# Kernel tuning notes

Hardware: AMD Instinct MI355X
Metric: run time of the kernel (lower is better)

Reference implementation:

```python
import jax, jax.numpy as jnp
import numpy as np

S_LOCAL = 3
N_HEADS = 8
EPS = 1e-6


def setup_inputs() -> dict:
    key = jax.random.key(0)
    ks = jax.random.split(key, 9)
    B, D, T, H, W = 2, 512, 96, 16, 16
    std = 0.02
    return {
        "x": jax.random.normal(ks[0], (B, D, T, H, W), dtype=jnp.float32),
        "ln_gamma": jnp.ones((D,), dtype=jnp.float32),
        "ln_beta": jnp.zeros((D,), dtype=jnp.float32),
        "Wq": jax.random.normal(ks[1], (D, D), dtype=jnp.float32) * std,
        "Wk": jax.random.normal(ks[2], (D, D), dtype=jnp.float32) * std,
        "Wv": jax.random.normal(ks[3], (D, D), dtype=jnp.float32) * std,
        "Wkl": jax.random.normal(ks[4], (D, D), dtype=jnp.float32) * std,
        "Wvl": jax.random.normal(ks[5], (D, D), dtype=jnp.float32) * std,
        "Wo": jax.random.normal(ks[6], (D, D), dtype=jnp.float32) * std,
        "q_bias": jax.random.normal(ks[7], (1, N_HEADS, 1, D // N_HEADS), dtype=jnp.float32) * std,
    }


def _unfold_windows(x, s):
    # x: [..., T] -> [..., T, s] sliding windows with zero padding s//2 each side
    p = s // 2
    xp = jnp.pad(x, [(0, 0)] * (x.ndim - 1) + [(p, p)])
    T = x.shape[-1]
    idx = jnp.arange(T)[:, None] + jnp.arange(s)[None, :]  # [T, s]
    return xp[..., idx]


def reference(x, ln_gamma, ln_beta, Wq, Wk, Wv, Wkl, Wvl, Wo, q_bias):
    B, D, T, H, W = x.shape
    nh, dh, s = N_HEADS, D // N_HEADS, S_LOCAL
    factor = dh ** (-0.5)
    N = B * H * W

    # [B,D,T,H,W] -> [N, T, D]
    xt = jnp.transpose(x, (0, 3, 4, 2, 1)).reshape(N, T, D)

    # LayerNorm over D
    mu = xt.mean(-1, keepdims=True)
    var = xt.var(-1, keepdims=True)
    xn = (xt - mu) / jnp.sqrt(var + EPS) * ln_gamma + ln_beta

    # projections -> [N, nh, T, dh]
    def heads(y):
        return jnp.transpose(y.reshape(N, T, nh, dh), (0, 2, 1, 3))

    q = heads(xn @ Wq.T) + q_bias
    k = heads(xn @ Wk.T)
    v = heads(xn @ Wv.T)

    # global attention scores [N, nh, T, T]
    attn_global = jnp.einsum('bhnd,bhgd->bhng', q, k) * factor

    # local k/v: [N, T, D] -> [N, D, T] -> windows [N, D, T, s]
    kl = jnp.transpose(xn @ Wkl.T, (0, 2, 1))
    vl = jnp.transpose(xn @ Wvl.T, (0, 2, 1))
    k_w = jnp.transpose(_unfold_windows(kl, s).reshape(N, nh, dh, T, s), (0, 1, 3, 2, 4))  # [N,nh,T,dh,s]
    v_w = jnp.transpose(_unfold_windows(vl, s).reshape(N, nh, dh, T, s), (0, 1, 3, 2, 4))

    # local mask: True where window element came from zero padding -> [T, s]
    mask_local = _unfold_windows(jnp.ones((T,), dtype=jnp.float32), s) == 0

    attn_local = jnp.einsum('bhnd,bhndl->bhnl', q, k_w)
    attn_local = jnp.where(mask_local, -jnp.inf, attn_local) * factor

    # joint softmax over [T global + s local]
    attn_map = jax.nn.softmax(jnp.concatenate([attn_global, attn_local], axis=-1), axis=-1)
    ag, al = attn_map[..., :T], attn_map[..., T:]

    x_global = jnp.einsum('bhng,bhgd->bhnd', ag, v)
    x_local = jnp.einsum('bhnl,bhndl->bhnd', al, v_w)

    out = (jnp.transpose(x_global + x_local, (0, 2, 1, 3)).reshape(N, T, D)) @ Wo.T
    return jnp.transpose(out.reshape(B, H, W, T, D), (0, 4, 3, 1, 2))
```

## Files before the change

kernel.cpp:

```cpp
#include <hip/hip_runtime.h>
#include <hip/hip_fp16.h>
#include <cstdint>
#include <cstddef>

typedef _Float16 f16;
typedef _Float16 half8 __attribute__((ext_vector_type(8)));
typedef _Float16 half4v __attribute__((ext_vector_type(4)));
typedef float floatx4 __attribute__((ext_vector_type(4)));

#define MTOT 49152

__device__ __forceinline__ void gload_lds16(const f16* g, f16* l) {
  __builtin_amdgcn_global_load_lds((const __attribute__((address_space(1))) void*)g,
                                   (__attribute__((address_space(3))) void*)l, 16, 0, 0);
}

__device__ __forceinline__ half8 load_h8u(const f16* p) {
  half8 v;
  __builtin_memcpy(&v, p, 16);
  return v;
}

__global__ __launch_bounds__(256) void wconv_kernel(
    const float* __restrict__ Wq, const float* __restrict__ Wk,
    const float* __restrict__ Wv, const float* __restrict__ Wkl,
    const float* __restrict__ Wvl, const float* __restrict__ Wo,
    f16* __restrict__ WQKV, f16* __restrict__ WO) {
  int idx = blockIdx.x * 256 + threadIdx.x;
  if (idx < 2560 * 512) {
    int row = idx >> 9;
    int col = idx & 511;
    int seg = row >> 9;
    int r = row & 511;
    const float* src;
    switch (seg) {
      case 0: src = Wq; break;
      case 1: src = Wk; break;
      case 2: src = Wkl; break;
      case 3: src = Wvl; break;
      default: src = Wv; break;
    }
    WQKV[idx] = (f16)src[r * 512 + col];
  }
  if (idx < 512 * 512) WO[idx] = (f16)Wo[idx];
}

__global__ __launch_bounds__(256) void ln_kernel(
    const float* __restrict__ x, const float* __restrict__ gamma,
    const float* __restrict__ beta, f16* __restrict__ XN) {
  const int hwg = blockIdx.x & 3;
  const int t   = (blockIdx.x >> 2) % 96;
  const int b   = blockIdx.x / (4 * 96);
  const int lhw = threadIdx.x & 63;
  const int dg  = threadIdx.x >> 6;
  const int hw  = hwg * 64 + lhw;
  const float* xp = x + (size_t)b * 512 * 24576 + (size_t)t * 256 + hw;

  float s = 0.f, s2 = 0.f;
  for (int d = dg * 128; d < dg * 128 + 128; ++d) {
    float v = xp[(size_t)d * 24576];
    s += v;
    s2 += v * v;
  }
  __shared__ float S1[4][64], S2[4][64];
  S1[dg][lhw] = s;
  S2[dg][lhw] = s2;
  __syncthreads();
  s  = S1[0][lhw] + S1[1][lhw] + S1[2][lhw] + S1[3][lhw];
  s2 = S2[0][lhw] + S2[1][lhw] + S2[2][lhw] + S2[3][lhw];
  const float mean = s * (1.f / 512.f);
  float var = s2 * (1.f / 512.f) - mean * mean;
  var = fmaxf(var, 0.f);
  const float rstd = rsqrtf(var + 1e-6f);
  const int n = b * 256 + hw;
  f16* outp = XN + ((size_t)n * 96 + t) * 512;
  for (int d0 = dg * 128; d0 < dg * 128 + 128; d0 += 8) {
    half8 buf;
#pragma unroll
    for (int j = 0; j < 8; ++j) {
      float v = xp[(size_t)(d0 + j) * 24576];
      buf[j] = (f16)((v - mean) * rstd * gamma[d0 + j] + beta[d0 + j]);
    }
    *(half8*)(outp + d0) = buf;
  }
}

__global__ __launch_bounds__(512, 2) void gemmA_kernel(
    const f16* __restrict__ A, const f16* __restrict__ B,
    f16* __restrict__ Cqkv, const float* __restrict__ qbias) {
  __shared__ f16 LA[2][256 * 64];
  __shared__ f16 LB[2][256 * 64];
  __shared__ __align__(16) f16 esc[8][16][72];

  const int lin = blockIdx.x;
  const int cpx = (int)gridDim.x >> 3;
  const int swz = (lin & 7) * cpx + (lin >> 3);
  const int o = ((gridDim.x & 7) == 0) ? swz : lin;
  const int mt = o / 10;
  const int nt = o % 10;
  const int m0 = mt * 256;
  const int n0 = nt * 256;

  const int tid = threadIdx.x;
  const int wid = tid >> 6;
  const int lane = tid & 63;
  const int wm = wid >> 2;
  const int wn = wid & 3;
  const int l15 = lane & 15, l4 = lane >> 4;

  const int srow = tid >> 3;
  const int scol = ((tid & 7) ^ (srow & 7)) * 8;
  const f16* Abase = A + (size_t)(m0 + srow) * 512 + scol;
  const f16* Bbase = B + (size_t)(n0 + srow) * 512 + scol;

  const int cks0 = ((l4) ^ (l15 & 7)) * 8;
  const int cks1 = ((4 + l4) ^ (l15 & 7)) * 8;
  const int arow = wm * 128 + l15;
  const int brow = wn * 64 + l15;

  floatx4 acc[8][4] = {};
  half8 a_f[4][2];
  half8 b_f[4][2];

  auto stageH = [&](int slot, int kt, int mat, int h) {
    const f16* g = (mat ? Bbase : Abase) + kt * 64 + (size_t)(h * 128) * 512;
    f16* l = (mat ? LB[slot] : LA[slot]) + h * 8192 + tid * 8;
    gload_lds16(g, l);
    gload_lds16(g + (size_t)64 * 512, l + 4096);
  };

  stageH(0, 0, 0, 0); stageH(0, 0, 0, 1);
  stageH(0, 0, 1, 0); stageH(0, 0, 1, 1);
  stageH(1, 1, 0, 0); stageH(1, 1, 0, 1);
  asm volatile("s_waitcnt vmcnt(4)" ::: "memory");
  __builtin_amdgcn_s_barrier();

#pragma unroll
  for (int kt = 0; kt < 8; ++kt) {
    const f16* As = LA[kt & 1];
    const f16* Bs = LB[kt & 1];
    const int nsl = (kt + 1) & 1;

#pragma unroll
    for (int mf2 = 0; mf2 < 4; ++mf2) {
      a_f[mf2][0] = *(const half8*)(As + (arow + mf2 * 16) * 64 + cks0);
      a_f[mf2][1] = *(const half8*)(As + (arow + mf2 * 16) * 64 + cks1);
    }
#pragma unroll
    for (int nf = 0; nf < 2; ++nf) {
      b_f[nf][0] = *(const half8*)(Bs + (brow + nf * 16) * 64 + cks0);
      b_f[nf][1] = *(const half8*)(Bs + (brow + nf * 16) * 64 + cks1);
    }
    if (kt + 1 < 8) { stageH(nsl, kt + 1, 1, 0); stageH(nsl, kt + 1, 1, 1); }
    __builtin_amdgcn_s_barrier();
    __builtin_amdgcn_s_setprio(1);
#pragma unroll
    for (int mf2 = 0; mf2 < 4; ++mf2)
#pragma unroll
      for (int nf2 = 0; nf2 < 2; ++nf2)
#pragma unroll
        for (int ks = 0; ks < 2; ++ks)
          acc[mf2][nf2] = __builtin_amdgcn_mfma_f32_16x16x32_f16(
              a_f[mf2][ks], b_f[nf2][ks], acc[mf2][nf2], 0, 0, 0);
    __builtin_amdgcn_s_setprio(0);
    __builtin_amdgcn_s_barrier();

#pragma unroll
    for (int nf = 2; nf < 4; ++nf) {
      b_f[nf][0] = *(const half8*)(Bs + (brow + nf * 16) * 64 + cks0);
      b_f[nf][1] = *(const half8*)(Bs + (brow + nf * 16) * 64 + cks1);
    }
    __builtin_amdgcn_s_barrier();
    __builtin_amdgcn_s_setprio(1);
#pragma unroll
    for (int mf2 = 0; mf2 < 4; ++mf2)
#pragma unroll
      for (int nf2 = 0; nf2 < 2; ++nf2)
#pragma unroll
        for (int ks = 0; ks < 2; ++ks)
          acc[mf2][2 + nf2] = __builtin_amdgcn_mfma_f32_16x16x32_f16(
              a_f[mf2][ks], b_f[2 + nf2][ks], acc[mf2][2 + nf2], 0, 0, 0);
    __builtin_amdgcn_s_setprio(0);
    __builtin_amdgcn_s_barrier();

#pragma unroll
    for (int mf2 = 0; mf2 < 4; ++mf2) {
      a_f[mf2][0] = *(const half8*)(As + (arow + 64 + mf2 * 16) * 64 + cks0);
      a_f[mf2][1] = *(const half8*)(As + (arow + 64 + mf2 * 16) * 64 + cks1);
    }
    __builtin_amdgcn_s_barrier();
    __builtin_amdgcn_s_setprio(1);
#pragma unroll
    for (int mf2 = 0; mf2 < 4; ++mf2)
#pragma unroll
      for (int nf2 = 0; nf2 < 2; ++nf2)
#pragma unroll
        for (int ks = 0; ks < 2; ++ks)
          acc[4 + mf2][nf2] = __builtin_amdgcn_mfma_f32_16x16x32_f16(
              a_f[mf2][ks], b_f[nf2][ks], acc[4 + mf2][nf2], 0, 0, 0);
    __builtin_amdgcn_s_setprio(0);
    __builtin_amdgcn_s_barrier();

    if (kt + 2 < 8) { stageH(kt & 1, kt + 2, 0, 0); stageH(kt & 1, kt + 2, 0, 1); }
    __builtin_amdgcn_s_barrier();
    __builtin_amdgcn_s_setprio(1);
#pragma unroll
    for (int mf2 = 0; mf2 < 4; ++mf2)
#pragma unroll
      for (int nf2 = 0; nf2 < 2; ++nf2)
#pragma unroll
        for (int ks = 0; ks < 2; ++ks)
          acc[4 + mf2][2 + nf2] = __builtin_amdgcn_mfma_f32_16x16x32_f16(
              a_f[mf2][ks], b_f[2 + nf2][ks], acc[4 + mf2][2 + nf2], 0, 0, 0);
    __builtin_amdgcn_s_setprio(0);
    if (kt < 6) {
      asm volatile("s_waitcnt vmcnt(4)" ::: "memory");
    } else if (kt == 6) {
      asm volatile("s_waitcnt vmcnt(0)" ::: "memory");
    }
    __builtin_amdgcn_s_barrier();
  }

  float bias[4], scl[4];
#pragma unroll
  for (int nf = 0; nf < 4; ++nf) {
    const int n = n0 + wn * 64 + nf * 16 + l15;
    const bool isq = (n < 512);
    bias[nf] = isq ? qbias[n] : 0.0f;
    scl[nf]  = isq ? 0.125f : 1.0f;
  }
  const int rrow = lane >> 2;
  const int rcg  = lane & 3;
#pragma unroll
  for (int mf = 0; mf < 8; ++mf) {
#pragma unroll
    for (int nf = 0; nf < 4; ++nf)
#pragma unroll
      for (int j = 0; j < 4; ++j)
        esc[wid][l4 * 4 + j][nf * 16 + l15] = (f16)((acc[mf][nf][j] + bias[nf]) * scl[nf]);
    asm volatile("s_waitcnt lgkmcnt(0)" ::: "memory");
    half8 v0 = *(const half8*)(&esc[wid][rrow][rcg * 16]);
    half8 v1 = *(const half8*)(&esc[wid][rrow][rcg * 16 + 8]);
    asm volatile("" ::: "memory");
    f16* dst = Cqkv + (size_t)(m0 + wm * 128 + mf * 16 + rrow) * 2560 + n0 + wn * 64 + rcg * 16;
    *(half8*)dst = v0;
    *(half8*)(dst + 8) = v1;
  }
}

__global__ __launch_bounds__(256) void gemmO_kernel(
    const f16* __restrict__ A, const f16* __restrict__ B,
    float* __restrict__ Out) {
  __shared__ f16 As[2][128 * 32];
  __shared__ f16 Bs[2][128 * 32];

  const int lin = blockIdx.x;
  const int cpx = (int)gridDim.x >> 3;
  const int o = (lin & 7) * cpx + (lin >> 3);
  const int nt = o >> 2;
  const int mt = o & 3;
  const int m0 = mt * 128;
  const int n0 = nt * 128;
  const int tid = threadIdx.x;
  const int lane = tid & 63;
  const int wid = tid >> 6;
  const int wm = wid >> 1, wn = wid & 1;
  const int l15 = lane & 15, l4 = lane >> 4;

  floatx4 acc[4][4] = {};

  const int srow = tid >> 2;
  const int skp = (((tid & 3) ^ ((tid >> 3) & 3))) * 8;
  const f16* ap = A + (size_t)(m0 + srow) * 512 + skp;
  const f16* bp = B + (size_t)(n0 + srow) * 512 + skp;

  auto stage = [&](int buf, int k0) {
    f16* asl = As[buf] + tid * 8;
    f16* bsl = Bs[buf] + tid * 8;
    gload_lds16(ap + k0, asl);
    gload_lds16(ap + (size_t)64 * 512 + k0, asl + 2048);
    gload_lds16(bp + k0, bsl);
    gload_lds16(bp + (size_t)64 * 512 + k0, bsl + 2048);
  };

  const int rc = (l4 ^ ((l15 >> 1) & 3)) * 8;

  stage(0, 0);
  __syncthreads();
  int cur = 0;
  for (int k0 = 0; k0 < 512; k0 += 32) {
    if (k0 + 32 < 512) stage(cur ^ 1, k0 + 32);
    half8 af[4], bf[4];
#pragma unroll
    for (int mf = 0; mf < 4; ++mf)
      af[mf] = *(const half8*)(As[cur] + (wm * 64 + mf * 16 + l15) * 32 + rc);
#pragma unroll
    for (int nf = 0; nf < 4; ++nf)
      bf[nf] = *(const half8*)(Bs[cur] + (wn * 64 + nf * 16 + l15) * 32 + rc);
#pragma unroll
    for (int mf = 0; mf < 4; ++mf)
#pragma unroll
      for (int nf = 0; nf < 4; ++nf)
        acc[mf][nf] = __builtin_amdgcn_mfma_f32_16x16x32_f16(af[mf], bf[nf], acc[mf][nf], 0, 0, 0);
    __syncthreads();
    cur ^= 1;
  }

  const int mbase = m0 + wm * 64;
  const int nbase = n0 + wn * 64;
#pragma unroll
  for (int nf = 0; nf < 4; ++nf) {
    const int m2 = nbase + nf * 16 + l15;
    const int bb = m2 / 24576;
    const int rem = m2 - bb * 24576;
    const int t = rem >> 8;
    const int hw = rem & 255;
    float* op = Out + ((size_t)bb * 512 * 96 + t) * 256 + hw;
#pragma unroll
    for (int mf = 0; mf < 4; ++mf) {
#pragma unroll
      for (int j = 0; j < 4; ++j) {
        const int d = mbase + mf * 16 + l4 * 4 + j;
        __builtin_nontemporal_store(acc[mf][nf][j], op + (size_t)d * 24576);
      }
    }
  }
}

__global__ __launch_bounds__(192) void attn_kernel(
    const f16* __restrict__ QKV, f16* __restrict__ AO, int n0chunk) {
  const int nn = blockIdx.x >> 3;
  const int h = blockIdx.x & 7;
  const int tid = threadIdx.x;
  const int wid = tid >> 6;
  const int lane = tid & 63;
  const int l15 = lane & 15, l4 = lane >> 4;
  const int nglob = n0chunk + nn;
  const int bb = nglob >> 8, hw = nglob & 255;

  __shared__ __align__(16) f16 VTl[64][112];
  __shared__ __align__(16) f16 VLTl[64][112];
  __shared__ __align__(16) float locS[3][16][4];
  __shared__ __align__(16) f16 pS[3][16][104];
  __shared__ __align__(16) f16 pS2[3][16][40];
  __shared__ __align__(16) f16 oesc[3][16][72];

  const f16* base = QKV + (size_t)nn * 96 * 2560;

#pragma unroll
  for (int it = 0; it < 4; ++it) {
    const int r = (tid >> 3) + it * 24;
    const int c0 = (tid & 7) * 8;
    half8 v  = *(const half8*)(base + (size_t)r * 2560 + 2048 + h * 64 + c0);
    half8 vl = *(const half8*)(base + (size_t)r * 2560 + 1536 + h * 64 + c0);
#pragma unroll
    for (int j = 0; j < 8; ++j) {
      VTl[c0 + j][r]  = v[j];
      VLTl[c0 + j][r] = vl[j];
    }
  }
  if (tid < 128) {
    half8 z = {};
    *(half8*)(&VLTl[tid >> 1][96 + (tid & 1) * 8]) = z;
  }

  half8 kb[6][2];
#pragma unroll
  for (int nf = 0; nf < 6; ++nf)
#pragma unroll
    for (int kg = 0; kg < 2; ++kg)
      kb[nf][kg] = *(const half8*)(base + (size_t)(nf * 16 + l15) * 2560 + 512 + h * 64 + kg * 32 + l4 * 8);

  __syncthreads();

  for (int mb = wid * 2; mb < wid * 2 + 2; ++mb) {
    const int t0 = mb * 16;
    const int tb = (t0 >= 2) ? (t0 - 2) : 0;
    const int d0 = t0 - 1 - tb;

    half8 aq[2], kl1[2], kl2[2];
    {
      int r1 = t0 - 1 + l15; if (r1 < 0) r1 = 0;
      int r2 = t0 + 1 + l15; if (r2 > 95) r2 = 95;
#pragma unroll
      for (int kg = 0; kg < 2; ++kg) {
        aq[kg]  = *(const half8*)(base + (size_t)(t0 + l15) * 2560 + h * 64 + kg * 32 + l4 * 8);
        kl1[kg] = *(const half8*)(base + (size_t)r1 * 2560 + 1024 + h * 64 + kg * 32 + l4 * 8);
        kl2[kg] = *(const half8*)(base + (size_t)r2 * 2560 + 1024 + h * 64 + kg * 32 + l4 * 8);
      }
    }

    floatx4 s[6] = {};
    floatx4 sl1 = {}, sl2 = {};
#pragma unroll
    for (int nf = 0; nf < 6; ++nf)
#pragma unroll
      for (int kg = 0; kg < 2; ++kg)
        s[nf] = __builtin_amdgcn_mfma_f32_16x16x32_f16(aq[kg], kb[nf][kg], s[nf], 0, 0, 0);
#pragma unroll
    for (int kg = 0; kg < 2; ++kg) {
      sl1 = __builtin_amdgcn_mfma_f32_16x16x32_f16(aq[kg], kl1[kg], sl1, 0, 0, 0);
      sl2 = __builtin_amdgcn_mfma_f32_16x16x32_f16(aq[kg], kl2[kg], sl2, 0, 0, 0);
    }

    half8 vb[4][3], vlb[4];
#pragma unroll
    for (int nf = 0; nf < 4; ++nf) {
#pragma unroll
      for (int kg = 0; kg < 3; ++kg)
        vb[nf][kg] = *(const half8*)(&VTl[nf * 16 + l15][kg * 32 + l4 * 8]);
      vlb[nf] = load_h8u(&VLTl[nf * 16 + l15][tb + l4 * 8]);
    }

    {
      half8 z = {};
      f16* pz = &pS2[wid][0][0];
      *(half8*)(pz + lane * 8) = z;
      if (lane < 16) *(half8*)(pz + 512 + lane * 8) = z;
    }
#pragma unroll
    for (int j = 0; j < 4; ++j) {
      const int r = l4 * 4 + j;
      const int s1i = l15 - r;
      if (s1i >= 0 && s1i < 3) locS[wid][r][s1i] = sl1[j];
      const int s2i = l15 + 2 - r;
      if (l15 >= 14 && s2i >= 0 && s2i < 3) locS[wid][r][s2i] = sl2[j];
    }
    __syncthreads();

#pragma unroll
    for (int j = 0; j < 4; ++j) {
      const int row = l4 * 4 + j;
      float sv[6];
#pragma unroll
      for (int nf = 0; nf < 6; ++nf) sv[nf] = s[nf][j];
      float mx = sv[0];
#pragma unroll
      for (int nf = 1; nf < 6; ++nf) mx = fmaxf(mx, sv[nf]);
      for (int off = 1; off < 16; off <<= 1) mx = fmaxf(mx, __shfl_xor(mx, off, 64));
      const float l0 = (t0 + row >= 1)  ? locS[wid][row][0] : -__builtin_inff();
      const float l1 = locS[wid][row][1];
      const float l2 = (t0 + row <= 94) ? locS[wid][row][2] : -__builtin_inff();
      mx = fmaxf(mx, fmaxf(l0, fmaxf(l1, l2)));
      float e[6], sum = 0.f;
#pragma unroll
      for (int nf = 0; nf < 6; ++nf) {
        e[nf] = expf(sv[nf] - mx);
        sum += e[nf];
      }
      for (int off = 1; off < 16; off <<= 1) sum += __shfl_xor(sum, off, 64);
      const float e0 = expf(l0 - mx), e1 = expf(l1 - mx), e2 = expf(l2 - mx);
      sum += e0 + e1 + e2;
      const float rd = 1.0f / sum;
#pragma unroll
      for (int nf = 0; nf < 6; ++nf) pS[wid][row][nf * 16 + l15] = (f16)(e[nf] * rd);
      if (l15 < 3) {
        const int w = row + l15 + d0;
        const float ev = (l15 == 0) ? e0 : ((l15 == 1) ? e1 : e2);
        if (w >= 0) pS2[wid][row][w] = (f16)(ev * rd);
      }
    }
    __syncthreads();

    floatx4 o[4] = {};
    half8 pfr[3];
#pragma unroll
    for (int kg = 0; kg < 3; ++kg)
      pfr[kg] = *(const half8*)(&pS[wid][l15][kg * 32 + l4 * 8]);
    half8 pf2 = *(const half8*)(&pS2[wid][l15][l4 * 8]);
#pragma unroll
    for (int nf = 0; nf < 4; ++nf) {
#pragma unroll
      for (int kg = 0; kg < 3; ++kg)
        o[nf] = __builtin_amdgcn_mfma_f32_16x16x32_f16(pfr[kg], vb[nf][kg], o[nf], 0, 0, 0);
      o[nf] = __builtin_amdgcn_mfma_f32_16x16x32_f16(pf2, vlb[nf], o[nf], 0, 0, 0);
    }

#pragma unroll
    for (int nf = 0; nf < 4; ++nf)
#pragma unroll
      for (int j = 0; j < 4; ++j)
        oesc[wid][l4 * 4 + j][nf * 16 + l15] = (f16)o[nf][j];
    asm volatile("s_waitcnt lgkmcnt(0)" ::: "memory");
    {
      const int rrow = lane >> 2;
      const int rcg  = lane & 3;
      half8 v0 = *(const half8*)(&oesc[wid][rrow][rcg * 16]);
      half8 v1 = *(const half8*)(&oesc[wid][rrow][rcg * 16 + 8]);
      asm volatile("" ::: "memory");
      f16* dst = AO + ((size_t)(bb * 96 + t0 + rrow) * 256 + hw) * 512 + h * 64 + rcg * 16;
      *(half8*)dst = v0;
      *(half8*)(dst + 8) = v1;
    }
  }
}

extern "C" void kernel_launch(void* const* d_in, const int* in_sizes, int n_in,
                              void* d_out, int out_size, void* d_ws, size_t ws_size,
                              hipStream_t stream) {
  (void)in_sizes; (void)n_in; (void)out_size;
  const float* x     = (const float*)d_in[0];
  const float* gamma = (const float*)d_in[1];
  const float* beta  = (const float*)d_in[2];
  const float* Wq    = (const float*)d_in[3];
  const float* Wk    = (const float*)d_in[4];
  const float* Wv    = (const float*)d_in[5];
  const float* Wkl   = (const float*)d_in[6];
  const float* Wvl   = (const float*)d_in[7];
  const float* Wo    = (const float*)d_in[8];
  const float* qb    = (const float*)d_in[9];
  float* out = (float*)d_out;

  char* ws = (char*)d_ws;
  size_t off = 0;
  auto alloc = [&](size_t bytes) -> void* {
    void* p = ws + off;
    off += (bytes + 255) & ~(size_t)255;
    return p;
  };
  f16* XN   = (f16*)alloc((size_t)MTOT * 512 * 2);
  f16* AO   = (f16*)alloc((size_t)MTOT * 512 * 2);
  f16* WQKV = (f16*)alloc((size_t)2560 * 512 * 2);
  f16* WOh  = (f16*)alloc((size_t)512 * 512 * 2);
  int cn = 512;
  while (cn > 32 && off + (size_t)cn * 96 * 2560 * 2 + 256 > ws_size)
    cn >>= 1;
  f16* QKVc = (f16*)alloc((size_t)cn * 96 * 2560 * 2);

  wconv_kernel<<<5120, 256, 0, stream>>>(Wq, Wk, Wv, Wkl, Wvl, Wo, WQKV, WOh);
  ln_kernel<<<768, 256, 0, stream>>>(x, gamma, beta, XN);

  const int nch = 512 / cn;
  for (int c = 0; c < nch; ++c) {
    const int mtiles = (cn * 96) / 256;
    gemmA_kernel<<<mtiles * 10, 512, 0, stream>>>(XN + (size_t)c * cn * 96 * 512,
                                                  WQKV, QKVc, qb);
    attn_kernel<<<cn * 8, 192, 0, stream>>>(QKVc, AO, c * cn);
  }
  gemmO_kernel<<<1536, 256, 0, stream>>>(WOh, AO, out);
}
```

Baseline: 426.2 us.

## Cache LN inputs in registers, spread GEMM staging, use exp2 softmax

LayerNorm now keeps all 128 per-thread values in registers, so x is read from global memory once instead of twice. The QKV GEMM spreads its global-to-LDS staging across the four MFMA phases (one half-tile per phase) and tightens the vmcnt waits to match, aiming for smoother load/compute overlap. Q is pre-scaled by log2(e)/sqrt(dh) so the softmax can use exp2f instead of expf. The 128-float register array raises register pressure in the LN kernel, and the reshuffled stage/wait ordering must stay consistent with the double buffering.

```diff
diff --git a/kernel.cpp b/kernel.cpp
--- a/kernel.cpp
+++ b/kernel.cpp
@@ -9,6 +9,7 @@
 typedef float floatx4 __attribute__((ext_vector_type(4)));
 
 #define MTOT 49152
+#define QSCALE 0.180336880111120426f
 
 __device__ __forceinline__ void gload_lds16(const f16* g, f16* l) {
   __builtin_amdgcn_global_load_lds((const __attribute__((address_space(1))) void*)g,
@@ -54,13 +55,17 @@
   const int lhw = threadIdx.x & 63;
   const int dg  = threadIdx.x >> 6;
   const int hw  = hwg * 64 + lhw;
-  const float* xp = x + (size_t)b * 512 * 24576 + (size_t)t * 256 + hw;
-
+  const float* xp = x + (size_t)b * 512 * 24576 + (size_t)t * 256 + hw +
+                    (size_t)dg * 128 * 24576;
+
+  float v[128];
   float s = 0.f, s2 = 0.f;
-  for (int d = dg * 128; d < dg * 128 + 128; ++d) {
-    float v = xp[(size_t)d * 24576];
-    s += v;
-    s2 += v * v;
+#pragma unroll
+  for (int j = 0; j < 128; ++j) {
+    float u = xp[(size_t)j * 24576];
+    v[j] = u;
+    s += u;
+    s2 += u * u;
   }
   __shared__ float S1[4][64], S2[4][64];
   S1[dg][lhw] = s;
@@ -73,13 +78,14 @@
   var = fmaxf(var, 0.f);
   const float rstd = rsqrtf(var + 1e-6f);
   const int n = b * 256 + hw;
-  f16* outp = XN + ((size_t)n * 96 + t) * 512;
-  for (int d0 = dg * 128; d0 < dg * 128 + 128; d0 += 8) {
+  f16* outp = XN + ((size_t)n * 96 + t) * 512 + dg * 128;
+#pragma unroll
+  for (int d0 = 0; d0 < 128; d0 += 8) {
     half8 buf;
 #pragma unroll
     for (int j = 0; j < 8; ++j) {
-      float v = xp[(size_t)(d0 + j) * 24576];
-      buf[j] = (f16)((v - mean) * rstd * gamma[d0 + j] + beta[d0 + j]);
+      const int d = dg * 128 + d0 + j;
+      buf[j] = (f16)((v[d0 + j] - mean) * rstd * gamma[d] + beta[d]);
     }
     *(half8*)(outp + d0) = buf;
   }
@@ -131,8 +137,8 @@
 
   stageH(0, 0, 0, 0); stageH(0, 0, 0, 1);
   stageH(0, 0, 1, 0); stageH(0, 0, 1, 1);
-  stageH(1, 1, 0, 0); stageH(1, 1, 0, 1);
-  asm volatile("s_waitcnt vmcnt(4)" ::: "memory");
+  stageH(1, 1, 0, 0);
+  asm volatile("s_waitcnt vmcnt(2)" ::: "memory");
   __builtin_amdgcn_s_barrier();
 
 #pragma unroll
@@ -151,7 +157,7 @@
       b_f[nf][0] = *(const half8*)(Bs + (brow + nf * 16) * 64 + cks0);
       b_f[nf][1] = *(const half8*)(Bs + (brow + nf * 16) * 64 + cks1);
     }
-    if (kt + 1 < 8) { stageH(nsl, kt + 1, 1, 0); stageH(nsl, kt + 1, 1, 1); }
+    if (kt + 1 < 8) stageH(nsl, kt + 1, 0, 1);
     __builtin_amdgcn_s_barrier();
     __builtin_amdgcn_s_setprio(1);
 #pragma unroll
@@ -170,6 +176,7 @@
       b_f[nf][0] = *(const half8*)(Bs + (brow + nf * 16) * 64 + cks0);
       b_f[nf][1] = *(const half8*)(Bs + (brow + nf * 16) * 64 + cks1);
     }
+    if (kt + 1 < 8) stageH(nsl, kt + 1, 1, 0);
     __builtin_amdgcn_s_barrier();
     __builtin_amdgcn_s_setprio(1);
 #pragma unroll
@@ -188,6 +195,7 @@
       a_f[mf2][0] = *(const half8*)(As + (arow + 64 + mf2 * 16) * 64 + cks0);
       a_f[mf2][1] = *(const half8*)(As + (arow + 64 + mf2 * 16) * 64 + cks1);
     }
+    if (kt + 1 < 8) stageH(nsl, kt + 1, 1, 1);
     __builtin_amdgcn_s_barrier();
     __builtin_amdgcn_s_setprio(1);
 #pragma unroll
@@ -201,7 +209,7 @@
     __builtin_amdgcn_s_setprio(0);
     __builtin_amdgcn_s_barrier();
 
-    if (kt + 2 < 8) { stageH(kt & 1, kt + 2, 0, 0); stageH(kt & 1, kt + 2, 0, 1); }
+    if (kt + 2 < 8) stageH(kt & 1, kt + 2, 0, 0);
     __builtin_amdgcn_s_barrier();
     __builtin_amdgcn_s_setprio(1);
 #pragma unroll
@@ -214,7 +222,7 @@
               a_f[mf2][ks], b_f[2 + nf2][ks], acc[4 + mf2][2 + nf2], 0, 0, 0);
     __builtin_amdgcn_s_setprio(0);
     if (kt < 6) {
-      asm volatile("s_waitcnt vmcnt(4)" ::: "memory");
+      asm volatile("s_waitcnt vmcnt(2)" ::: "memory");
     } else if (kt == 6) {
       asm volatile("s_waitcnt vmcnt(0)" ::: "memory");
     }
@@ -227,7 +235,7 @@
     const int n = n0 + wn * 64 + nf * 16 + l15;
     const bool isq = (n < 512);
     bias[nf] = isq ? qbias[n] : 0.0f;
-    scl[nf]  = isq ? 0.125f : 1.0f;
+    scl[nf]  = isq ? QSCALE : 1.0f;
   }
   const int rrow = lane >> 2;
   const int rcg  = lane & 3;
@@ -445,11 +453,11 @@
       float e[6], sum = 0.f;
 #pragma unroll
       for (int nf = 0; nf < 6; ++nf) {
-        e[nf] = expf(sv[nf] - mx);
+        e[nf] = exp2f(sv[nf] - mx);
         sum += e[nf];
       }
       for (int off = 1; off < 16; off <<= 1) sum += __shfl_xor(sum, off, 64);
-      const float e0 = expf(l0 - mx), e1 = expf(l1 - mx), e2 = expf(l2 - mx);
+      const float e0 = exp2f(l0 - mx), e1 = exp2f(l1 - mx), e2 = exp2f(l2 - mx);
       sum += e0 + e1 + e2;
       const float rd = 1.0f / sum;
 #pragma unroll
```

Measured after the change: 391.5 us, median of 2. -8.1%, faster.
